# Optimization experiments

Measured on AMD Instinct MI355X. Metric: run time of the kernel, lower is better.

## Reference

```python
import jax, jax.numpy as jnp
import numpy as np

D_MODEL = 2048
NUM_EXPERTS = 64
TOP_K = 2
N_TOKENS = 16384


def setup_inputs() -> dict:
    key = jax.random.key(0)
    kx, kw = jax.random.split(key)
    x = jax.random.normal(kx, (N_TOKENS, D_MODEL), dtype=jnp.float32)
    # match nn.Linear default init scale roughly (not bit-exact; math is what matters)
    W = jax.random.normal(kw, (D_MODEL, NUM_EXPERTS), dtype=jnp.float32) * (1.0 / np.sqrt(D_MODEL))
    b = jnp.zeros((NUM_EXPERTS,), dtype=jnp.float32)
    return {"x": x, "W": W, "b": b}


def reference(x, W, b):
    # eval-mode forward (self.training False => no noise)
    logits = jnp.einsum("td,de->te", x, W) + b          # [T, E]
    weights = jax.nn.softmax(logits, axis=-1)             # [T, E]
    topk_weights, topk_indices = jax.lax.top_k(weights, TOP_K)  # [T, k] each
    return topk_weights, topk_indices, weights
```

## Files before the change

kernel.cpp:

```cpp
#include <hip/hip_runtime.h>
#include <hip/hip_bf16.h>
#include <math.h>


#define T_TOK 16384
#define DMOD  2048
#define NEXP  64
#define NKSW  16
#define TOKB  32

typedef __attribute__((ext_vector_type(8))) short short8;
typedef __attribute__((ext_vector_type(4))) float f32x4;

#define MFMA16 __builtin_amdgcn_mfma_f32_16x16x32_bf16

__device__ __forceinline__ unsigned short bf16_rne(float f) {
  unsigned int u = __float_as_uint(f);
  unsigned int r = (u + 0x7fffu + ((u >> 16) & 1u)) >> 16;
  return (unsigned short)r;
}
__device__ __forceinline__ float bf16_up(unsigned short h) {
  return __uint_as_float(((unsigned int)h) << 16);
}
__device__ __forceinline__ unsigned short bf16_cvt(float f) {
  __hip_bfloat16 b = __float2bfloat16(f);
  return *reinterpret_cast<unsigned short*>(&b);
}

__device__ __forceinline__ void split3_pair(float v0, float v1, unsigned& hp,
                                            unsigned& mp, unsigned& lp) {
  const unsigned short h0 = bf16_rne(v0), h1 = bf16_rne(v1);
  const float e0 = v0 - bf16_up(h0), e1 = v1 - bf16_up(h1);
  const unsigned short m0 = bf16_rne(e0), m1 = bf16_rne(e1);
  const float g0 = e0 - bf16_up(m0), g1 = e1 - bf16_up(m1);
  const unsigned short l0 = bf16_rne(g0), l1 = bf16_rne(g1);
  hp = (unsigned)h0 | ((unsigned)h1 << 16);
  mp = (unsigned)m0 | ((unsigned)m1 << 16);
  lp = (unsigned)l0 | ((unsigned)l1 << 16);
}
__device__ __forceinline__ void split3_pair_hw(float v0, float v1,
                                               unsigned& hp, unsigned& mp,
                                               unsigned& lp) {
  const unsigned short h0 = bf16_cvt(v0), h1 = bf16_cvt(v1);
  const float e0 = v0 - bf16_up(h0), e1 = v1 - bf16_up(h1);
  const unsigned short m0 = bf16_cvt(e0), m1 = bf16_cvt(e1);
  const float g0 = e0 - bf16_up(m0), g1 = e1 - bf16_up(m1);
  const unsigned short l0 = bf16_cvt(g0), l1 = bf16_cvt(g1);
  hp = (unsigned)h0 | ((unsigned)h1 << 16);
  mp = (unsigned)m0 | ((unsigned)m1 << 16);
  lp = (unsigned)l0 | ((unsigned)l1 << 16);
}

__device__ __forceinline__ void glds16(const void* g, void* l) {
  __builtin_amdgcn_global_load_lds(
      (const __attribute__((address_space(1))) unsigned int*)g,
      (__attribute__((address_space(3))) unsigned int*)l, 16, 0, 0);
}

__global__ __launch_bounds__(64) void wconv_kernel(
    const float* __restrict__ W, unsigned short* __restrict__ wp) {
  const int tid = blockIdx.x * 64 + threadIdx.x;
  const int l = tid & 63;
  const int g = tid >> 6;
  const int q = l >> 4, c = l & 15;
  const int ks = g >> 2, nt = g & 3;
  const int k0 = ks * 32 + q * 8;
  const int n = nt * 16 + c;
  float v[8];
#pragma unroll
  for (int j = 0; j < 8; ++j) v[j] = W[(size_t)(k0 + j) * NEXP + n];
  uint4 h, m, lo;
  split3_pair(v[0], v[1], h.x, m.x, lo.x);
  split3_pair(v[2], v[3], h.y, m.y, lo.y);
  split3_pair(v[4], v[5], h.z, m.z, lo.z);
  split3_pair(v[6], v[7], h.w, m.w, lo.w);
  unsigned short* base = wp + (size_t)g * 1536 + l * 8;
  *(uint4*)(base) = h;
  *(uint4*)(base + 512) = m;
  *(uint4*)(base + 1024) = lo;
}

#define STAGE(D, KS)                                                  \
  do {                                                                \
    char* bd_ = bbuf + (D)*12288;                                     \
    const char* bs_ = wsrc + (size_t)(KS)*12288;                      \
    _Pragma("unroll") for (int i_ = 0; i_ < 12; ++i_)                 \
        glds16(bs_ + i_ * 1024, bd_ + i_ * 1024);                     \
    char* xd_ = xbuf + (D)*4096;                                      \
    const char* xs_ = xsrc + (size_t)(KS)*128;                        \
    _Pragma("unroll") for (int j_ = 0; j_ < 4; ++j_)                  \
        glds16(xs_ + j_ * 32, xd_ + j_ * 1024);                       \
    asm volatile("" ::: "memory");  \
  } while (0)

#define KSTEP(D, VM)                                                   \
  do {                                                                 \
    asm volatile("s_waitcnt vmcnt(" #VM ")" ::: "memory");             \
    const char* bd_ = bbuf + (D)*12288;                                \
    const char* xd_ = xbuf + (D)*4096;                                 \
    short8 bf[12];                                                     \
    _Pragma("unroll") for (int i_ = 0; i_ < 12; ++i_)                  \
        bf[i_] = *(const short8*)(bd_ + i_ * 1024 + l * 16);           \
    _Pragma("unroll") for (int mt_ = 0; mt_ < 2; ++mt_) {              \
      const int cb_ = (mt_ * 16 + c16) * 16;                           \
      const float4 xa = *(const float4*)(xd_ + q * 1024 + cb_);        \
      const float4 xb = *(const float4*)(xd_ + q * 1024 + 512 + cb_);  \
      uint4 h_, m_, lo_;                                               \
      split3_pair_hw(xa.x, xa.y, h_.x, m_.x, lo_.x);                   \
      split3_pair_hw(xa.z, xa.w, h_.y, m_.y, lo_.y);                   \
      split3_pair_hw(xb.x, xb.y, h_.z, m_.z, lo_.z);                   \
      split3_pair_hw(xb.z, xb.w, h_.w, m_.w, lo_.w);                   \
      const short8 ah = *(short8*)&h_;                                 \
      const short8 am = *(short8*)&m_;                                 \
      const short8 al = *(short8*)&lo_;                                \
      _Pragma("unroll") for (int nt_ = 0; nt_ < 4; ++nt_) {            \
        const short8 bh = bf[nt_ * 3 + 0];                             \
        const short8 bm = bf[nt_ * 3 + 1];                             \
        const short8 bl = bf[nt_ * 3 + 2];                             \
        acc[mt_][nt_] = MFMA16(ah, bh, acc[mt_][nt_], 0, 0, 0);        \
        acc[mt_][nt_] = MFMA16(ah, bm, acc[mt_][nt_], 0, 0, 0);        \
        acc[mt_][nt_] = MFMA16(am, bh, acc[mt_][nt_], 0, 0, 0);        \
        acc[mt_][nt_] = MFMA16(am, bm, acc[mt_][nt_], 0, 0, 0);        \
        acc[mt_][nt_] = MFMA16(ah, bl, acc[mt_][nt_], 0, 0, 0);        \
        acc[mt_][nt_] = MFMA16(al, bh, acc[mt_][nt_], 0, 0, 0);        \
      }                                                                \
    }                                                                  \
  } while (0)

__global__ __launch_bounds__(256, 1) void gating_kernel(
    const float* __restrict__ x, const unsigned short* __restrict__ wp,
    const float* __restrict__ bias, float* __restrict__ out) {
  __shared__ __align__(16) char smem[131072];

  const int tid = threadIdx.x;
  const int l = tid & 63;
  const int w = tid >> 6;
  const int q = l >> 4, c16 = l & 15;
  const int t0 = blockIdx.x * TOKB;

  char* bbuf = smem + w * 24576;
  char* xbuf = smem + 98304 + w * 8192;

  const char* wsrc = (const char*)wp + (size_t)(w * NKSW) * 12288 + l * 16;
  const char* xsrc = (const char*)x +
                     ((size_t)(t0 + (l & 31)) * DMOD + w * 512) * 4 +
                     (l >> 5) * 16;

  f32x4 acc[2][4];
#pragma unroll
  for (int mt = 0; mt < 2; ++mt)
#pragma unroll
    for (int nt = 0; nt < 4; ++nt) acc[mt][nt] = (f32x4){0.f, 0.f, 0.f, 0.f};

  STAGE(0, 0);
  STAGE(1, 1);

  for (int it = 0; it < 7; ++it) {
    KSTEP(0, 16);
    STAGE(0, 2 * it + 2);
    KSTEP(1, 16);
    STAGE(1, 2 * it + 3);
  }
  KSTEP(0, 16);
  KSTEP(1, 0);

  __syncthreads();
  float* partial = (float*)smem;
  float* red_m = partial + 8320;
  float* red_s = red_m + 32;
  float* lg = partial;

#pragma unroll
  for (int mt = 0; mt < 2; ++mt)
#pragma unroll
    for (int nt = 0; nt < 4; ++nt)
#pragma unroll
      for (int r = 0; r < 4; ++r)
        partial[w * 2080 + (mt * 16 + q * 4 + r) * 65 + nt * 16 + c16] =
            acc[mt][nt][r];
  __syncthreads();

#pragma unroll
  for (int r2 = 0; r2 < 8; ++r2) {
    const int idx = r2 * 256 + tid;
    const int tt = idx >> 6;
    const int e = idx & 63;
    const int o = tt * 65 + e;
    const float s = partial[o] + partial[2080 + o] + partial[4160 + o] +
                    partial[6240 + o];
    lg[o] = s + bias[e];
  }
  __syncthreads();

  if (tid < 128) {
    const int row = tid >> 2;
    const int s = tid & 3;
    const float* lr = lg + row * 65 + s * 16;
    float mx = -INFINITY;
#pragma unroll
    for (int e = 0; e < 16; ++e) mx = fmaxf(mx, lr[e]);
    mx = fmaxf(mx, __shfl_xor(mx, 1));
    mx = fmaxf(mx, __shfl_xor(mx, 2));
    float sum = 0.f, b1 = -INFINITY, b2 = -INFINITY;
    int i1 = 0, i2 = 0;
#pragma unroll
    for (int e = 0; e < 16; ++e) {
      const float v = lr[e];
      sum += expf(v - mx);
      const int idx = s * 16 + e;
      if (v > b1) {
        b2 = b1; i2 = i1; b1 = v; i1 = idx;
      } else if (v > b2) {
        b2 = v; i2 = idx;
      }
    }
#pragma unroll
    for (int msk = 1; msk <= 2; msk <<= 1) {
      sum += __shfl_xor(sum, msk);
      const float ob1 = __shfl_xor(b1, msk);
      const int oi1 = __shfl_xor(i1, msk);
      const float ob2 = __shfl_xor(b2, msk);
      const int oi2 = __shfl_xor(i2, msk);
      float n1, n2;
      int j1, j2;
      const bool aFirst = (b1 > ob1) || (b1 == ob1 && i1 < oi1);
      if (aFirst) {
        n1 = b1; j1 = i1;
        const bool t = (b2 > ob1) || (b2 == ob1 && i2 < oi1);
        n2 = t ? b2 : ob1; j2 = t ? i2 : oi1;
      } else {
        n1 = ob1; j1 = oi1;
        const bool t = (ob2 > b1) || (ob2 == b1 && oi2 < i1);
        n2 = t ? ob2 : b1; j2 = t ? oi2 : i1;
      }
      b1 = n1; i1 = j1; b2 = n2; i2 = j2;
    }
    if (s == 0) {
      const float inv = 1.f / sum;
      const int t = t0 + row;
      float2 wv, iv;
      wv.x = expf(b1 - mx) * inv;
      wv.y = expf(b2 - mx) * inv;
      iv.x = (float)i1;
      iv.y = (float)i2;
      *(float2*)(out + 2 * t) = wv;
      *(float2*)(out + 2 * T_TOK + 2 * t) = iv;
      red_m[row] = mx;
      red_s[row] = inv;
    }
  }
  __syncthreads();

#pragma unroll
  for (int r2 = 0; r2 < 8; ++r2) {
    const int idx = r2 * 256 + tid;
    const int tt = idx >> 6;
    const int e = idx & 63;
    out[4 * T_TOK + (size_t)(t0 + tt) * NEXP + e] =
        expf(lg[tt * 65 + e] - red_m[tt]) * red_s[tt];
  }
}

extern "C" void kernel_launch(void* const* d_in, const int* in_sizes, int n_in,
                              void* d_out, int out_size, void* d_ws,
                              size_t ws_size, hipStream_t stream) {
  const float* x = (const float*)d_in[0];
  const float* W = (const float*)d_in[1];
  const float* b = (const float*)d_in[2];
  float* out = (float*)d_out;
  unsigned short* wp = (unsigned short*)d_ws;
  wconv_kernel<<<dim3(256), dim3(64), 0, stream>>>(W, wp);
  gating_kernel<<<dim3(T_TOK / TOKB), dim3(256), 0, stream>>>(x, wp, b, out);
}
```

Measured before the change: 211.9 us.

## Double tokens per block to 64 to reuse staged weight tiles

Raises the token tile per workgroup from 32 to 64, so each staged weight slice feeds four M-tiles of MFMAs instead of two. This halves weight traffic per token and halves the grid to 256 blocks. The x staging layout is reworked and the shared buffer grows to 160KB, and the cross-wave reduction now has wave 0 sum the other waves' partials straight from its registers. The cost is more accumulator registers and fewer blocks in flight, which may reduce latency hiding. The weight-conversion kernel also moves from 64-thread to 256-thread blocks.

```diff
diff --git a/kernel.cpp b/kernel.cpp
--- a/kernel.cpp
+++ b/kernel.cpp
@@ -7,7 +7,7 @@
 #define DMOD  2048
 #define NEXP  64
 #define NKSW  16
-#define TOKB  32
+#define TOKB  64
 
 typedef __attribute__((ext_vector_type(8))) short short8;
 typedef __attribute__((ext_vector_type(4))) float f32x4;
@@ -57,9 +57,9 @@
       (__attribute__((address_space(3))) unsigned int*)l, 16, 0, 0);
 }
 
-__global__ __launch_bounds__(64) void wconv_kernel(
+__global__ __launch_bounds__(256) void wconv_kernel(
     const float* __restrict__ W, unsigned short* __restrict__ wp) {
-  const int tid = blockIdx.x * 64 + threadIdx.x;
+  const int tid = blockIdx.x * 256 + threadIdx.x;
   const int l = tid & 63;
   const int g = tid >> 6;
   const int q = l >> 4, c = l & 15;
@@ -80,57 +80,58 @@
   *(uint4*)(base + 1024) = lo;
 }
 
-#define STAGE(D, KS)                                                  \
-  do {                                                                \
-    char* bd_ = bbuf + (D)*12288;                                     \
-    const char* bs_ = wsrc + (size_t)(KS)*12288;                      \
-    _Pragma("unroll") for (int i_ = 0; i_ < 12; ++i_)                 \
-        glds16(bs_ + i_ * 1024, bd_ + i_ * 1024);                     \
-    char* xd_ = xbuf + (D)*4096;                                      \
-    const char* xs_ = xsrc + (size_t)(KS)*128;                        \
-    _Pragma("unroll") for (int j_ = 0; j_ < 4; ++j_)                  \
-        glds16(xs_ + j_ * 32, xd_ + j_ * 1024);                       \
+#define STAGE(D, KS)                                                   \
+  do {                                                                 \
+    char* bd_ = bbuf + (D)*12288;                                      \
+    const char* bs_ = wsrc + (size_t)(KS)*12288;                       \
+    _Pragma("unroll") for (int i_ = 0; i_ < 12; ++i_)                  \
+        glds16(bs_ + i_ * 1024, bd_ + i_ * 1024);                      \
+    char* xd_ = xbuf + (D)*8192;                                       \
+    const char* xs_ = xsrc + (size_t)(KS)*128;                         \
+    _Pragma("unroll") for (int j_ = 0; j_ < 8; ++j_)                   \
+        glds16(xs_ + j_ * 16, xd_ + j_ * 1024);                        \
     asm volatile("" ::: "memory");  \
   } while (0)
 
-#define KSTEP(D, VM)                                                   \
-  do {                                                                 \
-    asm volatile("s_waitcnt vmcnt(" #VM ")" ::: "memory");             \
-    const char* bd_ = bbuf + (D)*12288;                                \
-    const char* xd_ = xbuf + (D)*4096;                                 \
-    short8 bf[12];                                                     \
-    _Pragma("unroll") for (int i_ = 0; i_ < 12; ++i_)                  \
-        bf[i_] = *(const short8*)(bd_ + i_ * 1024 + l * 16);           \
-    _Pragma("unroll") for (int mt_ = 0; mt_ < 2; ++mt_) {              \
-      const int cb_ = (mt_ * 16 + c16) * 16;                           \
-      const float4 xa = *(const float4*)(xd_ + q * 1024 + cb_);        \
-      const float4 xb = *(const float4*)(xd_ + q * 1024 + 512 + cb_);  \
-      uint4 h_, m_, lo_;                                               \
-      split3_pair_hw(xa.x, xa.y, h_.x, m_.x, lo_.x);                   \
-      split3_pair_hw(xa.z, xa.w, h_.y, m_.y, lo_.y);                   \
-      split3_pair_hw(xb.x, xb.y, h_.z, m_.z, lo_.z);                   \
-      split3_pair_hw(xb.z, xb.w, h_.w, m_.w, lo_.w);                   \
-      const short8 ah = *(short8*)&h_;                                 \
-      const short8 am = *(short8*)&m_;                                 \
-      const short8 al = *(short8*)&lo_;                                \
-      _Pragma("unroll") for (int nt_ = 0; nt_ < 4; ++nt_) {            \
-        const short8 bh = bf[nt_ * 3 + 0];                             \
-        const short8 bm = bf[nt_ * 3 + 1];                             \
-        const short8 bl = bf[nt_ * 3 + 2];                             \
-        acc[mt_][nt_] = MFMA16(ah, bh, acc[mt_][nt_], 0, 0, 0);        \
-        acc[mt_][nt_] = MFMA16(ah, bm, acc[mt_][nt_], 0, 0, 0);        \
-        acc[mt_][nt_] = MFMA16(am, bh, acc[mt_][nt_], 0, 0, 0);        \
-        acc[mt_][nt_] = MFMA16(am, bm, acc[mt_][nt_], 0, 0, 0);        \
-        acc[mt_][nt_] = MFMA16(ah, bl, acc[mt_][nt_], 0, 0, 0);        \
-        acc[mt_][nt_] = MFMA16(al, bh, acc[mt_][nt_], 0, 0, 0);        \
-      }                                                                \
-    }                                                                  \
+#define KSTEP(D, VM)                                                    \
+  do {                                                                  \
+    asm volatile("s_waitcnt vmcnt(" #VM ")" ::: "memory");              \
+    const char* bd_ = bbuf + (D)*12288;                                 \
+    const char* xd_ = xbuf + (D)*8192;                                  \
+    short8 bf[12];                                                      \
+    _Pragma("unroll") for (int i_ = 0; i_ < 12; ++i_)                   \
+        bf[i_] = *(const short8*)(bd_ + i_ * 1024 + l * 16);            \
+    _Pragma("unroll") for (int mt_ = 0; mt_ < 4; ++mt_) {               \
+      const int tok_ = mt_ * 16 + c16;                                  \
+      const float4 xa = *(const float4*)(xd_ + q * 2048 + tok_ * 16);   \
+      const float4 xb =                                                 \
+          *(const float4*)(xd_ + q * 2048 + 1024 + tok_ * 16);          \
+      uint4 h_, m_, lo_;                                                \
+      split3_pair_hw(xa.x, xa.y, h_.x, m_.x, lo_.x);                    \
+      split3_pair_hw(xa.z, xa.w, h_.y, m_.y, lo_.y);                    \
+      split3_pair_hw(xb.x, xb.y, h_.z, m_.z, lo_.z);                    \
+      split3_pair_hw(xb.z, xb.w, h_.w, m_.w, lo_.w);                    \
+      const short8 ah = *(short8*)&h_;                                  \
+      const short8 am = *(short8*)&m_;                                  \
+      const short8 al = *(short8*)&lo_;                                 \
+      _Pragma("unroll") for (int nt_ = 0; nt_ < 4; ++nt_) {             \
+        const short8 bh = bf[nt_ * 3 + 0];                              \
+        const short8 bm = bf[nt_ * 3 + 1];                              \
+        const short8 bl = bf[nt_ * 3 + 2];                              \
+        acc[mt_][nt_] = MFMA16(ah, bh, acc[mt_][nt_], 0, 0, 0);         \
+        acc[mt_][nt_] = MFMA16(ah, bm, acc[mt_][nt_], 0, 0, 0);         \
+        acc[mt_][nt_] = MFMA16(am, bh, acc[mt_][nt_], 0, 0, 0);         \
+        acc[mt_][nt_] = MFMA16(am, bm, acc[mt_][nt_], 0, 0, 0);         \
+        acc[mt_][nt_] = MFMA16(ah, bl, acc[mt_][nt_], 0, 0, 0);         \
+        acc[mt_][nt_] = MFMA16(al, bh, acc[mt_][nt_], 0, 0, 0);         \
+      }                                                                 \
+    }                                                                   \
   } while (0)
 
 __global__ __launch_bounds__(256, 1) void gating_kernel(
     const float* __restrict__ x, const unsigned short* __restrict__ wp,
     const float* __restrict__ bias, float* __restrict__ out) {
-  __shared__ __align__(16) char smem[131072];
+  __shared__ __align__(16) char smem[163840];
 
   const int tid = threadIdx.x;
   const int l = tid & 63;
@@ -139,16 +140,15 @@
   const int t0 = blockIdx.x * TOKB;
 
   char* bbuf = smem + w * 24576;
-  char* xbuf = smem + 98304 + w * 8192;
+  char* xbuf = smem + 98304 + w * 16384;
 
   const char* wsrc = (const char*)wp + (size_t)(w * NKSW) * 12288 + l * 16;
-  const char* xsrc = (const char*)x +
-                     ((size_t)(t0 + (l & 31)) * DMOD + w * 512) * 4 +
-                     (l >> 5) * 16;
-
-  f32x4 acc[2][4];
-#pragma unroll
-  for (int mt = 0; mt < 2; ++mt)
+  const char* xsrc =
+      (const char*)x + ((size_t)(t0 + l) * DMOD + w * 512) * 4;
+
+  f32x4 acc[4][4];
+#pragma unroll
+  for (int mt = 0; mt < 4; ++mt)
 #pragma unroll
     for (int nt = 0; nt < 4; ++nt) acc[mt][nt] = (f32x4){0.f, 0.f, 0.f, 0.f};
 
@@ -156,43 +156,49 @@
   STAGE(1, 1);
 
   for (int it = 0; it < 7; ++it) {
-    KSTEP(0, 16);
+    KSTEP(0, 20);
     STAGE(0, 2 * it + 2);
-    KSTEP(1, 16);
+    KSTEP(1, 20);
     STAGE(1, 2 * it + 3);
   }
-  KSTEP(0, 16);
+  KSTEP(0, 20);
   KSTEP(1, 0);
 
   __syncthreads();
   float* partial = (float*)smem;
-  float* red_m = partial + 8320;
-  float* red_s = red_m + 32;
+  float* red_m = partial + 12480;
+  float* red_s = partial + 12544;
   float* lg = partial;
 
-#pragma unroll
-  for (int mt = 0; mt < 2; ++mt)
-#pragma unroll
-    for (int nt = 0; nt < 4; ++nt)
-#pragma unroll
-      for (int r = 0; r < 4; ++r)
-        partial[w * 2080 + (mt * 16 + q * 4 + r) * 65 + nt * 16 + c16] =
-            acc[mt][nt][r];
-  __syncthreads();
-
-#pragma unroll
-  for (int r2 = 0; r2 < 8; ++r2) {
-    const int idx = r2 * 256 + tid;
-    const int tt = idx >> 6;
-    const int e = idx & 63;
-    const int o = tt * 65 + e;
-    const float s = partial[o] + partial[2080 + o] + partial[4160 + o] +
-                    partial[6240 + o];
-    lg[o] = s + bias[e];
-  }
-  __syncthreads();
-
-  if (tid < 128) {
+  if (w > 0) {
+    float* pp = partial + (w - 1) * 4160;
+#pragma unroll
+    for (int mt = 0; mt < 4; ++mt)
+#pragma unroll
+      for (int nt = 0; nt < 4; ++nt)
+#pragma unroll
+        for (int r = 0; r < 4; ++r)
+          pp[(mt * 16 + q * 4 + r) * 65 + nt * 16 + c16] = acc[mt][nt][r];
+  }
+  __syncthreads();
+
+  if (w == 0) {
+#pragma unroll
+    for (int mt = 0; mt < 4; ++mt)
+#pragma unroll
+      for (int nt = 0; nt < 4; ++nt) {
+        const float bv = bias[nt * 16 + c16];
+#pragma unroll
+        for (int r = 0; r < 4; ++r) {
+          const int o = (mt * 16 + q * 4 + r) * 65 + nt * 16 + c16;
+          lg[o] = ((acc[mt][nt][r] + partial[o]) + partial[4160 + o]) +
+                  partial[8320 + o] + bv;
+        }
+      }
+  }
+  __syncthreads();
+
+  {
     const int row = tid >> 2;
     const int s = tid & 3;
     const float* lr = lg + row * 65 + s * 16;
@@ -252,7 +258,7 @@
   __syncthreads();
 
 #pragma unroll
-  for (int r2 = 0; r2 < 8; ++r2) {
+  for (int r2 = 0; r2 < 16; ++r2) {
     const int idx = r2 * 256 + tid;
     const int tt = idx >> 6;
     const int e = idx & 63;
@@ -269,6 +275,6 @@
   const float* b = (const float*)d_in[2];
   float* out = (float*)d_out;
   unsigned short* wp = (unsigned short*)d_ws;
-  wconv_kernel<<<dim3(256), dim3(64), 0, stream>>>(W, wp);
+  wconv_kernel<<<dim3(64), dim3(256), 0, stream>>>(W, wp);
   gating_kernel<<<dim3(T_TOK / TOKB), dim3(256), 0, stream>>>(x, wp, b, out);
 }
```

Result: no change. 209.4 us (-1.1%).
